# Optimization experiments

Measured on AMD Instinct MI355X. Metric: run time of the kernel, lower is better.

## Reference

```python
import jax, jax.numpy as jnp
import numpy as np

MAXDISP = 320
NEG_SLOPE = 0.2


def _lrelu(x):
    return jnp.where(x >= 0, x, NEG_SLOPE * x)


def _conv(x, w, b, stride):
    # NCHW conv, VALID padding (torch Conv2d with padding=0)
    y = jax.lax.conv_general_dilated(x, w, window_strides=stride, padding='VALID',
                                     dimension_numbers=('NCHW', 'OIHW', 'NCHW'))
    return y + b[None, :, None, None]


def _tile_pair(fl, fr, wa, ba, wb, bb):
    # left: 4x4 conv stride (4,4); right: ZeroPad2d((0,3,0,0)) then stride (4,1)
    tl = _lrelu(_conv(_lrelu(_conv(fl, wa, ba, (4, 4))), wb, bb, (1, 1)))
    frp = jnp.pad(fr, ((0, 0), (0, 0), (0, 0), (0, 3)))
    tr = _lrelu(_conv(_lrelu(_conv(frp, wa, ba, (4, 1))), wb, bb, (1, 1)))
    return tl, tr


def _calc_init_disp(fl, fr, D):
    # fl: [B,C,h,w4], fr: [B,C,h,w] with w = 4*w4.
    # grid_sample(nearest, align_corners=True) with integer coords reduces to
    # exact gather at right column index 4*j - d, zero outside (padding_mode=zeros).
    B, C, h, w4 = fl.shape
    w = fr.shape[3]
    j = jnp.arange(w4)
    d = jnp.arange(D)
    idx = 4 * j[None, :] - d[:, None]              # [D, w4]
    valid = idx >= 0                               # only left edge can go OOB
    idxc = jnp.clip(idx, 0, w - 1)
    fr_g = fr[:, :, :, idxc]                       # [B,C,h,D,w4]
    fr_g = jnp.where(valid[None, None, None, :, :], fr_g, jnp.zeros((), fr.dtype))
    cv = jnp.abs(fl[:, :, :, None, :] - fr_g).sum(axis=1)  # L1 over C -> [B,h,D,w4]
    return jnp.transpose(cv, (0, 2, 1, 3))         # [B,D,h,w4]


def _level_hyp(cv, dscrpt_feat, dw, db):
    min_cost = jnp.min(cv, axis=1, keepdims=True)
    disp = jnp.argmin(cv, axis=1, keepdims=True).astype(cv.dtype)
    dscrpt = _lrelu(_conv(jnp.concatenate([min_cost, dscrpt_feat], axis=1), dw, db, (1, 1)))
    z = jnp.zeros_like(disp)
    return jnp.concatenate([disp, z, z, dscrpt], axis=1)  # [B,16,h,w]


def setup_inputs() -> dict:
    key = jax.random.key(0)
    ks = iter(jax.random.split(key, 64))

    def rn(shape, s=1.0):
        return jax.random.normal(next(ks), shape, dtype=jnp.float32) * s

    B, H, W = 1, 384, 1280
    inp = {
        'fea_l16': rn((B, 32, H // 16, W // 16)), 'fea_l8': rn((B, 24, H // 8, W // 8)),
        'fea_l4': rn((B, 24, H // 4, W // 4)), 'fea_l2': rn((B, 16, H // 2, W // 2)),
        'fea_l1': rn((B, 16, H, W)),
        'fea_r16': rn((B, 32, H // 16, W // 16)), 'fea_r8': rn((B, 24, H // 8, W // 8)),
        'fea_r4': rn((B, 24, H // 4, W // 4)), 'fea_r2': rn((B, 16, H // 2, W // 2)),
        'fea_r1': rn((B, 16, H, W)),
    }
    fea_c = {16: 32, 8: 24, 4: 24, 2: 16, 1: 16}
    for s, c in fea_c.items():
        inp[f'tcw{s}a'] = rn((16, c, 4, 4), 0.1)
        inp[f'tcb{s}a'] = rn((16,), 0.1)
        inp[f'tcw{s}b'] = rn((16, 16, 1, 1), 0.1)
        inp[f'tcb{s}b'] = rn((16,), 0.1)
    dsc_in = {16: 17, 8: 17, 4: 33, 2: 25, 1: 25}
    for s, c in dsc_in.items():
        inp[f'dw{s}'] = rn((13, c, 1, 1), 0.1)
        inp[f'db{s}'] = rn((13,), 0.1)
    return inp


def reference(fea_l16, fea_l8, fea_l4, fea_l2, fea_l1,
              fea_r16, fea_r8, fea_r4, fea_r2, fea_r1,
              tcw16a, tcb16a, tcw16b, tcb16b,
              tcw8a, tcb8a, tcw8b, tcb8b,
              tcw4a, tcb4a, tcw4b, tcb4b,
              tcw2a, tcb2a, tcw2b, tcb2b,
              tcw1a, tcb1a, tcw1b, tcb1b,
              dw16, db16, dw8, db8, dw4, db4, dw2, db2, dw1, db1):
    tl16, tr16 = _tile_pair(fea_l16, fea_r16, tcw16a, tcb16a, tcw16b, tcb16b)
    tl8, tr8 = _tile_pair(fea_l8, fea_r8, tcw8a, tcb8a, tcw8b, tcb8b)
    tl4, tr4 = _tile_pair(fea_l4, fea_r4, tcw4a, tcb4a, tcw4b, tcb4b)
    tl2, tr2 = _tile_pair(fea_l2, fea_r2, tcw2a, tcb2a, tcw2b, tcb2b)
    tl1, tr1 = _tile_pair(fea_l1, fea_r1, tcw1a, tcb1a, tcw1b, tcb1b)

    cv16 = _calc_init_disp(tl16, tr16, MAXDISP // 16)
    cv8 = _calc_init_disp(tl8, tr8, MAXDISP // 8)
    cv4 = _calc_init_disp(tl4, tr4, MAXDISP // 4)
    cv2 = _calc_init_disp(tl2, tr2, MAXDISP // 2)
    cv1 = _calc_init_disp(tl1, tr1, MAXDISP)

    hyp16 = _level_hyp(cv16, tl16, dw16, db16)
    hyp8 = _level_hyp(cv8, tl8, dw8, db8)
    hyp4 = _level_hyp(cv4, fea_l16, dw4, db4)
    hyp2 = _level_hyp(cv2, fea_l8, dw2, db2)
    hyp1 = _level_hyp(cv1, fea_l4, dw1, db1)

    return (cv16, cv8, cv4, cv2, cv1, hyp16, hyp8, hyp4, hyp2, hyp1)
```

## Files before the change

### kernel.cpp

```cpp
#include <hip/hip_runtime.h>
#include <float.h>

#define NEG_SLOPE 0.2f

__device__ __forceinline__ float lrelu(float x) { return x >= 0.0f ? x : NEG_SLOPE * x; }

struct ConvSeg {
    const float* in; const float* wa; const float* wb; const float* ba; const float* bb;
    float* out;
    int CIN, H, W, right, OW, cw, nchunk, npix, blk0;
};
struct ConvTab { ConvSeg seg[10]; };

#define STR 1028

__global__ __launch_bounds__(256)
void conv_uber(ConvTab tab) {
    __shared__ float s_in[2 * 4 * STR];
    __shared__ float s_w[2 * 256];
    __shared__ float s_wb[256];
    __shared__ float s_ba[16], s_bb[16];

    int si = 0;
#pragma unroll
    for (int i = 1; i < 10; i++) if ((int)blockIdx.x >= tab.seg[i].blk0) si = i;
    const ConvSeg sg = tab.seg[si];
    const int CIN = sg.CIN, W = sg.W, OW = sg.OW;
    const int tid = threadIdx.x;

    const int rel = (int)blockIdx.x - sg.blk0;
    const int y = rel / sg.nchunk, chk = rel - y * sg.nchunk;
    const int ox0 = chk * sg.cw;
    const int cwo = min(sg.cw, OW - ox0);
    const bool valid = tid < cwo;

    s_wb[tid] = sg.wb[(tid & 15) * 16 + (tid >> 4)];
    if (tid < 16) { s_ba[tid] = sg.ba[tid]; s_bb[tid] = sg.bb[tid]; }

    const size_t HW = (size_t)sg.H * W;
    const float* inb = sg.in + (size_t)(4 * y) * W;
    const int cbase = sg.right ? ox0 : 4 * ox0;
    const int span = cwo + 3;

    s_w[tid] = sg.wa[(tid & 15) * (CIN * 16) + (tid >> 4)];
    if (sg.right) {
        for (int cc = tid; cc < span; cc += 256) {
            int gc = cbase + cc;
#pragma unroll
            for (int rr = 0; rr < 4; rr++)
                s_in[rr * STR + cc] = (gc < W) ? inb[rr * W + gc] : 0.f;
        }
    } else {
        for (int j = tid; j < cwo; j += 256) {
#pragma unroll
            for (int rr = 0; rr < 4; rr++)
                *(float4*)&s_in[rr * STR + 4 * j] = *(const float4*)&inb[rr * W + cbase + 4 * j];
        }
    }
    __syncthreads();

    float m[16];
#pragma unroll
    for (int co = 0; co < 16; co++) m[co] = 0.f;

    int buf = 0;
    for (int c = 0; c < CIN; c++) {
        const int nb = buf ^ 1;
        if (c + 1 < CIN) {
            s_w[nb * 256 + tid] = sg.wa[(tid & 15) * (CIN * 16) + (c + 1) * 16 + (tid >> 4)];
            const float* inc = inb + (size_t)(c + 1) * HW;
            if (sg.right) {
                for (int cc = tid; cc < span; cc += 256) {
                    int gc = cbase + cc;
#pragma unroll
                    for (int rr = 0; rr < 4; rr++)
                        s_in[nb * 4 * STR + rr * STR + cc] = (gc < W) ? inc[rr * W + gc] : 0.f;
                }
            } else {
                for (int j = tid; j < cwo; j += 256) {
#pragma unroll
                    for (int rr = 0; rr < 4; rr++)
                        *(float4*)&s_in[nb * 4 * STR + rr * STR + 4 * j] =
                            *(const float4*)&inc[rr * W + cbase + 4 * j];
                }
            }
        }
        if (valid) {
            const float* sb = s_in + buf * 4 * STR;
            float wv[16];
            if (sg.right) {
#pragma unroll
                for (int rr = 0; rr < 4; rr++)
#pragma unroll
                    for (int k = 0; k < 4; k++) wv[rr * 4 + k] = sb[rr * STR + tid + k];
            } else {
#pragma unroll
                for (int rr = 0; rr < 4; rr++) {
                    float4 f = *(const float4*)&sb[rr * STR + 4 * tid];
                    wv[rr * 4 + 0] = f.x; wv[rr * 4 + 1] = f.y;
                    wv[rr * 4 + 2] = f.z; wv[rr * 4 + 3] = f.w;
                }
            }
            const float* wc = s_w + buf * 256;
#pragma unroll
            for (int tap = 0; tap < 16; tap++) {
                float v = wv[tap];
                const float* w2 = wc + tap * 16;
#pragma unroll
                for (int co = 0; co < 16; co++) m[co] = fmaf(v, w2[co], m[co]);
            }
        }
        __syncthreads();
        buf = nb;
    }

    if (valid) {
#pragma unroll
        for (int co = 0; co < 16; co++) m[co] = lrelu(m[co] + s_ba[co]);
        float o[16];
#pragma unroll
        for (int co = 0; co < 16; co++) o[co] = 0.f;
#pragma unroll
        for (int k = 0; k < 16; k++) {
            float mk = m[k];
            const float* wr = s_wb + k * 16;
#pragma unroll
            for (int co = 0; co < 16; co++) o[co] = fmaf(mk, wr[co], o[co]);
        }
        const int op = y * OW + ox0 + tid;
#pragma unroll
        for (int co = 0; co < 16; co++)
            sg.out[(size_t)co * sg.npix + op] = lrelu(o[co] + s_bb[co]);
    }
}

struct CvSeg {
    const float* tl; const float* tr; const float* feat;
    const float* dw; const float* db;
    float* cv; float* hyp;
    int h, w4, w, D, gpc, CF, blk0;
};
struct CvTab { CvSeg seg[5]; };

__global__ __launch_bounds__(256)
void cv_hyp_uber(CvTab tab) {
    __shared__ float smin[256];
    __shared__ int sarg[256];

    int si = 0;
#pragma unroll
    for (int i = 1; i < 5; i++) if ((int)blockIdx.x >= tab.seg[i].blk0) si = i;
    const CvSeg sg = tab.seg[si];

    const int npix = sg.h * sg.w4;
    const int p = threadIdx.x & 15, chunk = threadIdx.x >> 4;
    const int pix = ((int)blockIdx.x - sg.blk0) * 16 + p;
    const bool valid = pix < npix;

    float mloc = FLT_MAX; int aloc = 0;
    if (valid) {
        int y = pix / sg.w4, j = pix - y * sg.w4;
        float tlv[16]; float sumabs = 0.f;
#pragma unroll
        for (int c = 0; c < 16; c++) { tlv[c] = sg.tl[(size_t)c * npix + pix]; sumabs += fabsf(tlv[c]); }

        int ngroups = sg.D >> 2;
        int g0 = chunk * sg.gpc;
        int g1 = min(ngroups, g0 + sg.gpc);
        const float* trrow = sg.tr + (size_t)y * sg.w;
        int hw = sg.h * sg.w;

        float carry[16];
        int b0 = 4 * j - 4 * g0;
        if (g0 < g1 && b0 >= 0) {
#pragma unroll
            for (int c = 0; c < 16; c++) carry[c] = trrow[(size_t)c * hw + b0];
        }
        for (int g = g0; g < g1; g++) {
            int b = 4 * j - 4 * g;
            float a0, a1, a2, a3;
            if (b >= 4) {
                a0 = a1 = a2 = a3 = 0.f;
#pragma unroll
                for (int c = 0; c < 16; c++) {
                    float4 f0 = *(const float4*)(trrow + (size_t)c * hw + (b - 4));
                    float tv = tlv[c];
                    a0 += fabsf(tv - carry[c]);
                    a1 += fabsf(tv - f0.w);
                    a2 += fabsf(tv - f0.z);
                    a3 += fabsf(tv - f0.y);
                    carry[c] = f0.x;
                }
            } else if (b == 0) {
                a0 = 0.f; a1 = a2 = a3 = sumabs;
#pragma unroll
                for (int c = 0; c < 16; c++) a0 += fabsf(tlv[c] - carry[c]);
            } else {
                a0 = a1 = a2 = a3 = sumabs;
            }
            float* cvp = sg.cv + (size_t)(4 * g) * npix + pix;
            cvp[0] = a0; cvp[npix] = a1; cvp[2 * (size_t)npix] = a2; cvp[3 * (size_t)npix] = a3;
            if (a0 < mloc) { mloc = a0; aloc = 4 * g; }
            if (a1 < mloc) { mloc = a1; aloc = 4 * g + 1; }
            if (a2 < mloc) { mloc = a2; aloc = 4 * g + 2; }
            if (a3 < mloc) { mloc = a3; aloc = 4 * g + 3; }
        }
    }
    smin[threadIdx.x] = mloc;
    sarg[threadIdx.x] = aloc;
    __syncthreads();

    if (threadIdx.x < 16 && valid) {
        float mn = smin[threadIdx.x]; int arg = sarg[threadIdx.x];
#pragma unroll
        for (int c2 = 1; c2 < 16; c2++) {
            float v = smin[c2 * 16 + threadIdx.x];
            if (v < mn) { mn = v; arg = sarg[c2 * 16 + threadIdx.x]; }
        }
        float acc[13];
#pragma unroll
        for (int o = 0; o < 13; o++) acc[o] = sg.dw[o * (sg.CF + 1)] * mn;
        for (int c = 0; c < sg.CF; c++) {
            float v = sg.feat[(size_t)c * npix + pix];
#pragma unroll
            for (int o = 0; o < 13; o++) acc[o] = fmaf(v, sg.dw[o * (sg.CF + 1) + 1 + c], acc[o]);
        }
        sg.hyp[pix] = (float)arg;
        sg.hyp[npix + pix] = 0.f;
        sg.hyp[2 * (size_t)npix + pix] = 0.f;
#pragma unroll
        for (int o = 0; o < 13; o++) sg.hyp[(size_t)(3 + o) * npix + pix] = lrelu(acc[o] + sg.db[o]);
    }
}

extern "C" void kernel_launch(void* const* d_in, const int* in_sizes, int n_in,
                              void* d_out, int out_size, void* d_ws, size_t ws_size,
                              hipStream_t stream) {
    (void)in_sizes; (void)n_in; (void)out_size; (void)ws_size;
    float* out = (float*)d_out;
    float* ws = (float*)d_ws;

    const int C[5] = {32, 24, 24, 16, 16};
    const int H[5] = {24, 48, 96, 192, 384};
    const int W[5] = {80, 160, 320, 640, 1280};
    const int D[5] = {20, 40, 80, 160, 320};
    const int wa_i[5] = {10, 14, 18, 22, 26};
    const int dw_i[5] = {30, 32, 34, 36, 38};

    const size_t cv_off[5]  = {0, 2400, 21600, 175200, 1404000};
    const size_t hyp_off[5] = {11234400, 11236320, 11244000, 11274720, 11397600};
    const size_t tl_off[5] = {0, 9600, 48000, 201600, 816000};
    const size_t tr_off[5] = {1920, 17280, 78720, 324480, 1307520};

    const float* fl[5] = {(const float*)d_in[0], (const float*)d_in[1], (const float*)d_in[2],
                          (const float*)d_in[3], (const float*)d_in[4]};
    const float* fr[5] = {(const float*)d_in[5], (const float*)d_in[6], (const float*)d_in[7],
                          (const float*)d_in[8], (const float*)d_in[9]};

    const int ord_lvl[10]  = {4, 4, 3, 3, 2, 2, 1, 1, 0, 0};
    const int ord_side[10] = {1, 0, 1, 0, 1, 0, 1, 0, 1, 0};
    ConvTab ct;
    int blk = 0;
    for (int i = 0; i < 10; i++) {
        int l = ord_lvl[i]; bool right = ord_side[i];
        ConvSeg& s = ct.seg[i];
        s.in = right ? fr[l] : fl[l];
        s.wa = (const float*)d_in[wa_i[l]];
        s.ba = (const float*)d_in[wa_i[l] + 1];
        s.wb = (const float*)d_in[wa_i[l] + 2];
        s.bb = (const float*)d_in[wa_i[l] + 3];
        s.out = ws + (right ? tr_off[l] : tl_off[l]);
        s.CIN = C[l]; s.H = H[l]; s.W = W[l];
        s.right = right ? 1 : 0;
        int OH = H[l] / 4;
        s.OW = right ? W[l] : W[l] / 4;
        s.nchunk = (s.OW + 255) / 256;
        s.cw = (s.OW + s.nchunk - 1) / s.nchunk;
        s.npix = OH * s.OW;
        s.blk0 = blk;
        blk += OH * s.nchunk;
    }
    conv_uber<<<blk, 256, 0, stream>>>(ct);

    const float* feat[5] = {ws + tl_off[0], ws + tl_off[1], fl[0], fl[1], fl[2]};
    const int   CF[5]    = {16, 16, 32, 24, 24};
    CvTab vt;
    blk = 0;
    for (int i = 0; i < 5; i++) {
        int l = 4 - i;
        CvSeg& s = vt.seg[i];
        s.tl = ws + tl_off[l]; s.tr = ws + tr_off[l];
        s.feat = feat[l];
        s.dw = (const float*)d_in[dw_i[l]];
        s.db = (const float*)d_in[dw_i[l] + 1];
        s.cv = out + cv_off[l]; s.hyp = out + hyp_off[l];
        s.h = H[l] / 4; s.w4 = W[l] / 4; s.w = W[l]; s.D = D[l];
        int ngroups = D[l] / 4;
        s.gpc = (ngroups + 15) / 16;
        s.CF = CF[l];
        s.blk0 = blk;
        blk += (s.h * s.w4 + 15) / 16;
    }
    cv_hyp_uber<<<blk, 256, 0, stream>>>(vt);
}
```

Baseline: 338.5 us.

## Retile conv_uber: per-wave output-channel groups, register prefetch, LDS transpose epilogue

Changes how work in the first conv stage is split across threads. Each wave now computes 4 output channels for 4 pixels, reading float4 weight vectors from LDS. For the right (stride-1) side, overlapping input windows are reused in registers. The next channel's input is prefetched into registers before the compute and written to LDS afterwards, so global latency overlaps the FMAs. Intermediate activations are then transposed through LDS back to a one-pixel-per-thread layout for the 1x1 conv. Chunk width is rounded up to a multiple of 4. The intent is to cut LDS traffic and idle threads, at the cost of more registers and an extra barrier.

```diff
diff --git a/kernel.cpp b/kernel.cpp
--- a/kernel.cpp
+++ b/kernel.cpp
@@ -12,12 +12,12 @@
 };
 struct ConvTab { ConvSeg seg[10]; };
 
-#define STR 1028
+#define SROW 1040
 
 __global__ __launch_bounds__(256)
 void conv_uber(ConvTab tab) {
-    __shared__ float s_in[2 * 4 * STR];
-    __shared__ float s_w[2 * 256];
+    __shared__ float s_in[2][4][SROW];
+    __shared__ float s_w[2][256];
     __shared__ float s_wb[256];
     __shared__ float s_ba[16], s_bb[16];
 
@@ -26,13 +26,13 @@
     for (int i = 1; i < 10; i++) if ((int)blockIdx.x >= tab.seg[i].blk0) si = i;
     const ConvSeg sg = tab.seg[si];
     const int CIN = sg.CIN, W = sg.W, OW = sg.OW;
-    const int tid = threadIdx.x;
+    const int tid = threadIdx.x, lane = tid & 63;
+    const int cb = (tid >> 6) * 4;
 
     const int rel = (int)blockIdx.x - sg.blk0;
     const int y = rel / sg.nchunk, chk = rel - y * sg.nchunk;
     const int ox0 = chk * sg.cw;
     const int cwo = min(sg.cw, OW - ox0);
-    const bool valid = tid < cwo;
 
     s_wb[tid] = sg.wb[(tid & 15) * 16 + (tid >> 4)];
     if (tid < 16) { s_ba[tid] = sg.ba[tid]; s_bb[tid] = sg.bb[tid]; }
@@ -42,91 +42,144 @@
     const int cbase = sg.right ? ox0 : 4 * ox0;
     const int span = cwo + 3;
 
-    s_w[tid] = sg.wa[(tid & 15) * (CIN * 16) + (tid >> 4)];
+    s_w[0][tid] = sg.wa[(tid & 15) * (CIN * 16) + (tid >> 4)];
     if (sg.right) {
         for (int cc = tid; cc < span; cc += 256) {
             int gc = cbase + cc;
 #pragma unroll
-            for (int rr = 0; rr < 4; rr++)
-                s_in[rr * STR + cc] = (gc < W) ? inb[rr * W + gc] : 0.f;
-        }
-    } else {
-        for (int j = tid; j < cwo; j += 256) {
-#pragma unroll
-            for (int rr = 0; rr < 4; rr++)
-                *(float4*)&s_in[rr * STR + 4 * j] = *(const float4*)&inb[rr * W + cbase + 4 * j];
-        }
+            for (int r = 0; r < 4; r++)
+                s_in[0][r][cc] = (gc < W) ? inb[r * W + gc] : 0.f;
+        }
+    } else if (tid < cwo) {
+#pragma unroll
+        for (int r = 0; r < 4; r++)
+            *(float4*)&s_in[0][r][4 * tid] = *(const float4*)&inb[r * W + cbase + 4 * tid];
     }
     __syncthreads();
 
-    float m[16];
-#pragma unroll
-    for (int co = 0; co < 16; co++) m[co] = 0.f;
+    float m[4][4];
+#pragma unroll
+    for (int i = 0; i < 4; i++)
+#pragma unroll
+        for (int q = 0; q < 4; q++) m[i][q] = 0.f;
 
     int buf = 0;
     for (int c = 0; c < CIN; c++) {
         const int nb = buf ^ 1;
-        if (c + 1 < CIN) {
-            s_w[nb * 256 + tid] = sg.wa[(tid & 15) * (CIN * 16) + (c + 1) * 16 + (tid >> 4)];
+        float rw = 0.f, rs[16];
+        const bool more = (c + 1 < CIN);
+        if (more) {
+            rw = sg.wa[(tid & 15) * (CIN * 16) + (c + 1) * 16 + (tid >> 4)];
             const float* inc = inb + (size_t)(c + 1) * HW;
             if (sg.right) {
-                for (int cc = tid; cc < span; cc += 256) {
-                    int gc = cbase + cc;
-#pragma unroll
-                    for (int rr = 0; rr < 4; rr++)
-                        s_in[nb * 4 * STR + rr * STR + cc] = (gc < W) ? inc[rr * W + gc] : 0.f;
+                int gc = cbase + tid;
+#pragma unroll
+                for (int r = 0; r < 4; r++)
+                    rs[r] = (tid < span && gc < W) ? inc[r * W + gc] : 0.f;
+                int gc2 = cbase + tid + 256;
+#pragma unroll
+                for (int r = 0; r < 4; r++)
+                    rs[4 + r] = (tid + 256 < span && gc2 < W) ? inc[r * W + gc2] : 0.f;
+            } else if (tid < cwo) {
+#pragma unroll
+                for (int r = 0; r < 4; r++) {
+                    float4 f = *(const float4*)&inc[r * W + cbase + 4 * tid];
+                    rs[4 * r] = f.x; rs[4 * r + 1] = f.y; rs[4 * r + 2] = f.z; rs[4 * r + 3] = f.w;
                 }
-            } else {
-                for (int j = tid; j < cwo; j += 256) {
-#pragma unroll
-                    for (int rr = 0; rr < 4; rr++)
-                        *(float4*)&s_in[nb * 4 * STR + rr * STR + 4 * j] =
-                            *(const float4*)&inc[rr * W + cbase + 4 * j];
+            }
+        }
+        if (sg.right) {
+#pragma unroll
+            for (int r = 0; r < 4; r++) {
+                float4 a = *(const float4*)&s_in[buf][r][4 * lane];
+                float4 b = *(const float4*)&s_in[buf][r][4 * lane + 4];
+                float v[8] = {a.x, a.y, a.z, a.w, b.x, b.y, b.z, b.w};
+#pragma unroll
+                for (int kx = 0; kx < 4; kx++) {
+                    float4 wq = *(const float4*)&s_w[buf][(r * 4 + kx) * 16 + cb];
+#pragma unroll
+                    for (int i = 0; i < 4; i++) {
+                        float vv = v[i + kx];
+                        m[i][0] = fmaf(vv, wq.x, m[i][0]);
+                        m[i][1] = fmaf(vv, wq.y, m[i][1]);
+                        m[i][2] = fmaf(vv, wq.z, m[i][2]);
+                        m[i][3] = fmaf(vv, wq.w, m[i][3]);
+                    }
                 }
             }
-        }
-        if (valid) {
-            const float* sb = s_in + buf * 4 * STR;
-            float wv[16];
+        } else {
+#pragma unroll
+            for (int i = 0; i < 4; i++) {
+                if (64 * i >= cwo) break;
+                const int col = 4 * (lane + 64 * i);
+                float4 q0 = *(const float4*)&s_in[buf][0][col];
+                float4 q1 = *(const float4*)&s_in[buf][1][col];
+                float4 q2 = *(const float4*)&s_in[buf][2][col];
+                float4 q3 = *(const float4*)&s_in[buf][3][col];
+                float qa[16] = {q0.x, q0.y, q0.z, q0.w, q1.x, q1.y, q1.z, q1.w,
+                                q2.x, q2.y, q2.z, q2.w, q3.x, q3.y, q3.z, q3.w};
+#pragma unroll
+                for (int tap = 0; tap < 16; tap++) {
+                    float4 wq = *(const float4*)&s_w[buf][tap * 16 + cb];
+                    float vv = qa[tap];
+                    m[i][0] = fmaf(vv, wq.x, m[i][0]);
+                    m[i][1] = fmaf(vv, wq.y, m[i][1]);
+                    m[i][2] = fmaf(vv, wq.z, m[i][2]);
+                    m[i][3] = fmaf(vv, wq.w, m[i][3]);
+                }
+            }
+        }
+        if (more) {
+            s_w[nb][tid] = rw;
             if (sg.right) {
-#pragma unroll
-                for (int rr = 0; rr < 4; rr++)
-#pragma unroll
-                    for (int k = 0; k < 4; k++) wv[rr * 4 + k] = sb[rr * STR + tid + k];
-            } else {
-#pragma unroll
-                for (int rr = 0; rr < 4; rr++) {
-                    float4 f = *(const float4*)&sb[rr * STR + 4 * tid];
-                    wv[rr * 4 + 0] = f.x; wv[rr * 4 + 1] = f.y;
-                    wv[rr * 4 + 2] = f.z; wv[rr * 4 + 3] = f.w;
-                }
-            }
-            const float* wc = s_w + buf * 256;
-#pragma unroll
-            for (int tap = 0; tap < 16; tap++) {
-                float v = wv[tap];
-                const float* w2 = wc + tap * 16;
-#pragma unroll
-                for (int co = 0; co < 16; co++) m[co] = fmaf(v, w2[co], m[co]);
+                if (tid < span)
+#pragma unroll
+                    for (int r = 0; r < 4; r++) s_in[nb][r][tid] = rs[r];
+                if (tid + 256 < span)
+#pragma unroll
+                    for (int r = 0; r < 4; r++) s_in[nb][r][tid + 256] = rs[4 + r];
+            } else if (tid < cwo) {
+#pragma unroll
+                for (int r = 0; r < 4; r++)
+                    *(float4*)&s_in[nb][r][4 * tid] =
+                        make_float4(rs[4 * r], rs[4 * r + 1], rs[4 * r + 2], rs[4 * r + 3]);
             }
         }
         __syncthreads();
         buf = nb;
     }
 
-    if (valid) {
-#pragma unroll
-        for (int co = 0; co < 16; co++) m[co] = lrelu(m[co] + s_ba[co]);
-        float o[16];
-#pragma unroll
-        for (int co = 0; co < 16; co++) o[co] = 0.f;
-#pragma unroll
-        for (int k = 0; k < 16; k++) {
-            float mk = m[k];
-            const float* wr = s_wb + k * 16;
-#pragma unroll
-            for (int co = 0; co < 16; co++) o[co] = fmaf(mk, wr[co], o[co]);
-        }
+    float* x_lds = &s_in[0][0][0];
+    if (sg.right) {
+#pragma unroll
+        for (int q = 0; q < 4; q++)
+            *(float4*)&x_lds[(cb + q) * 256 + 4 * lane] =
+                make_float4(m[0][q], m[1][q], m[2][q], m[3][q]);
+    } else {
+#pragma unroll
+        for (int i = 0; i < 4; i++) {
+            if (64 * i >= cwo) break;
+#pragma unroll
+            for (int q = 0; q < 4; q++)
+                x_lds[(cb + q) * 256 + lane + 64 * i] = m[i][q];
+        }
+    }
+    __syncthreads();
+
+    float x[16];
+#pragma unroll
+    for (int k = 0; k < 16; k++) x[k] = lrelu(x_lds[k * 256 + tid] + s_ba[k]);
+    float o[16];
+#pragma unroll
+    for (int co = 0; co < 16; co++) o[co] = 0.f;
+#pragma unroll
+    for (int k = 0; k < 16; k++) {
+        float mk = x[k];
+        const float* wr = s_wb + k * 16;
+#pragma unroll
+        for (int co = 0; co < 16; co++) o[co] = fmaf(mk, wr[co], o[co]);
+    }
+    if (tid < cwo) {
         const int op = y * OW + ox0 + tid;
 #pragma unroll
         for (int co = 0; co < 16; co++)
@@ -275,7 +328,8 @@
         int OH = H[l] / 4;
         s.OW = right ? W[l] : W[l] / 4;
         s.nchunk = (s.OW + 255) / 256;
-        s.cw = (s.OW + s.nchunk - 1) / s.nchunk;
+        int cwr = (s.OW + s.nchunk - 1) / s.nchunk;
+        s.cw = (cwr + 3) & ~3;
         s.npix = OH * s.OW;
         s.blk0 = blk;
         blk += OH * s.nchunk;
```

Result: faster. 315.9 us (-6.7%).
